# Performance work log

Measured on AMD Instinct MI355X. Metric: run time of the kernel, lower is better.

Reference implementation:

```python
import jax, jax.numpy as jnp
import numpy as np
from jax import lax

B, C, H, G = 128, 512, 14, 20  # batch, channels, feature-map size, num branches

# landmark indices for (point1, point2) of the 10 regions, and y-offset coefficients (x ruler)
_I1 = jnp.array([21, 18, 19, 41, 38, 49, 48, 51, 61, 56])
_I2 = jnp.array([22, 25, 24, 46, 43, 53, 54, 57, 63, 58])
_COEF = jnp.array([-0.5, -1.0 / 3.0, 1.0 / 3.0, 1.0, 0.0, 0.0, 0.0, 0.0, 0.0, 0.5], jnp.float32)


def process_landmarks(y):
    # y: [B,68,2] (x,y) pixel coords -> region_array [B,10,4] = (x1,y1,x2,y2)/16
    xl, yl = y[:, :, 0], y[:, :, 1]
    ruler = jnp.abs(xl[:, 39] - xl[:, 42])            # [B]
    off = ruler[:, None] * _COEF[None, :]             # [B,10]
    region = jnp.stack([xl[:, _I1], yl[:, _I1] + off, xl[:, _I2], yl[:, _I2] + off], axis=-1)
    return region / 16.0


def _crop(xi, cyi, cxi):
    # xi: [C,H,W]; 3x3 window centered at (cyi, cxi)
    z = jnp.asarray(0, cyi.dtype)
    return lax.dynamic_slice(xi, (z, cyi - 1, cxi - 1), (C, 3, 3))


def setup_inputs() -> dict:
    key = jax.random.key(0)
    ks = jax.random.split(key, 4)
    x = jax.random.normal(ks[0], (B, C, H, H), jnp.float32)
    y = jax.random.uniform(ks[1], (B, 68, 2), jnp.float32) * 224.0
    conv_w = jax.random.normal(ks[2], (G * C, C, 3, 3), jnp.float32) * 0.02  # grouped OIHW
    conv_b = jnp.zeros((G * C,), jnp.float32)
    fc_w = jax.random.normal(ks[3], (G, C * 36, 150), jnp.float32) * 0.01
    fc_b = jnp.zeros((G, 150), jnp.float32)
    return {"x": x, "y": y, "conv_w": conv_w, "conv_b": conv_b, "fc_w": fc_w, "fc_b": fc_b}


def reference(x, y, conv_w, conv_b, fc_w, fc_b):
    bsz = x.shape[0]
    pos = jnp.clip(process_landmarks(y).astype(jnp.int32), 1, 12)   # [B,10,4]
    cx = pos[:, :, jnp.array([0, 2])].reshape(bsz, G)               # [B,20] cols
    cy = pos[:, :, jnp.array([1, 3])].reshape(bsz, G)               # [B,20] rows
    crops = jax.vmap(jax.vmap(_crop, in_axes=(None, 0, 0)), in_axes=(0, 0, 0))(x, cy, cx)  # [B,20,C,3,3]
    new_input = crops.reshape(bsz, G * C, 3, 3)
    up = jax.image.resize(new_input, (bsz, G * C, 6, 6), method='bilinear')  # half-pixel, matches torch align_corners=False
    conv = lax.conv_general_dilated(up, conv_w, (1, 1), ((1, 1), (1, 1)),
                                    feature_group_count=G,
                                    dimension_numbers=('NCHW', 'OIHW', 'NCHW'))
    conv = jax.nn.relu(conv + conv_b[None, :, None, None])          # [B, G*C, 6, 6]
    feat = conv.reshape(bsz, G, C * 36)
    fc = jax.nn.relu(jnp.einsum('bgi,gio->bgo', feat, fc_w) + fc_b[None])  # [B,G,150]
    return fc.reshape(bsz, G * 150)
```

## Files before the change

### kernel.cpp

```cpp
#include <hip/hip_runtime.h>
#include <stdint.h>

#define B_  128
#define C_  512
#define G_  20
#define K2  4608
#define FCK 18432

typedef unsigned short u16;
typedef unsigned int   u32;
typedef __attribute__((ext_vector_type(8))) short  short8;
typedef __attribute__((ext_vector_type(4))) short  short4v;
typedef __attribute__((ext_vector_type(4))) float  float4v;

__device__ __forceinline__ u16 f2bf(float f) {
  u32 u = __builtin_bit_cast(u32, f);
  u = (u + 0x7fffu + ((u >> 16) & 1u)) >> 16;
  return (u16)u;
}

__device__ __forceinline__ void load_lds16(const void* g, void* l) {
  __builtin_amdgcn_global_load_lds(
      (const __attribute__((address_space(1))) void*)(uintptr_t)g,
      (__attribute__((address_space(3))) void*)(uint32_t)(uintptr_t)l,
      16, 0, 0);
}

#define BAR() __builtin_amdgcn_s_barrier()

__global__ void k_pos(const float* __restrict__ y, int* __restrict__ cx, int* __restrict__ cy) {
  int b = blockIdx.x * blockDim.x + threadIdx.x;
  if (b >= B_) return;
  const int   I1[10] = {21,18,19,41,38,49,48,51,61,56};
  const int   I2[10] = {22,25,24,46,43,53,54,57,63,58};
  const float CF[10] = {-0.5f, -1.0f/3.0f, 1.0f/3.0f, 1.0f, 0.f,0.f,0.f,0.f,0.f, 0.5f};
  const float* yb = y + b * 136;
  float ruler = fabsf(yb[2*39] - yb[2*42]);
  for (int j = 0; j < 10; ++j) {
    float off = ruler * CF[j];
    float vx1 = yb[2*I1[j]];
    float vy1 = yb[2*I1[j]+1] + off;
    float vx2 = yb[2*I2[j]];
    float vy2 = yb[2*I2[j]+1] + off;
    int px1 = (int)(vx1 * 0.0625f); px1 = min(max(px1,1),12);
    int py1 = (int)(vy1 * 0.0625f); py1 = min(max(py1,1),12);
    int px2 = (int)(vx2 * 0.0625f); px2 = min(max(px2,1),12);
    int py2 = (int)(vy2 * 0.0625f); py2 = min(max(py2,1),12);
    cx[b*20 + 2*j]   = px1;  cx[b*20 + 2*j+1] = px2;
    cy[b*20 + 2*j]   = py1;  cy[b*20 + 2*j+1] = py2;
  }
}

__global__ void __launch_bounds__(256) k_convw(const float* __restrict__ w, u16* __restrict__ wb) {
  __shared__ u16 lds[4 * 4608];
  int ob = blockIdx.x * 4;
  int tid = threadIdx.x;
  const float4* in4 = (const float4*)(w + (size_t)ob * 4608);
  #pragma unroll
  for (int r = 0; r < 18; ++r) {
    int fi = r * 256 + tid;
    float4 v = in4[fi];
    u16 q[4] = { f2bf(v.x), f2bf(v.y), f2bf(v.z), f2bf(v.w) };
    *(short4v*)&lds[fi * 4] = *(short4v*)q;
  }
  __syncthreads();
  #pragma unroll
  for (int r = 0; r < 9; ++r) {
    int wi = r * 256 + tid;
    int ci0 = (wi & 63) * 8;
    int t   = (wi >> 6) % 9;
    int o   = wi / 576;
    u16 vals[8];
    #pragma unroll
    for (int j = 0; j < 8; ++j) vals[j] = lds[o * 4608 + (ci0 + j) * 9 + t];
    *(short8*)(wb + ((size_t)(ob + o)) * K2 + t * 512 + ci0) = *(short8*)vals;
  }
}

__global__ void __launch_bounds__(256) k_up3(const float* __restrict__ x,
                                             const int* __restrict__ cx,
                                             const int* __restrict__ cy,
                                             u16* __restrict__ up3) {
  __shared__ float crop[3][3][C_];
  int bg = blockIdx.x;
  int b = bg / 20, g = bg % 20;
  int X = cx[bg] - 1, Y = cy[bg] - 1;
  const float* xb = x + (size_t)b * (C_*14*14);
  int t = threadIdx.x;
  for (int it = 0; it < 6; ++it) {
    int idx = it*256 + t;
    int r = idx >> 9, ci = idx & 511;
    const float* srow = xb + ci*196 + (Y + r)*14 + X;
    crop[r][0][ci] = srow[0];
    crop[r][1][ci] = srow[1];
    crop[r][2][ci] = srow[2];
  }
  __syncthreads();
  const int   R0[6] = {0,0,0,1,1,1};
  const float WA[6] = {1.f, .75f, .25f, .75f, .25f, 0.f};
  u16* dstbase = up3 + ((size_t)g*B_ + b) * 64 * C_;
  for (int it = 0; it < 16; ++it) {
    int cidx = it*256 + t;
    int pp = cidx >> 6;
    int c8 = (cidx & 63) * 8;
    int ph = pp >> 3, pw = pp & 7;
    u16 outv[8];
    if (ph == 0 || ph == 7 || pw == 0 || pw == 7) {
      #pragma unroll
      for (int j = 0; j < 8; ++j) outv[j] = 0;
    } else {
      int oh = ph - 1, ow = pw - 1;
      int r0 = R0[oh]; float wy0 = WA[oh], wy1 = 1.f - WA[oh];
      int s0 = R0[ow]; float wx0 = WA[ow], wx1 = 1.f - WA[ow];
      #pragma unroll
      for (int j = 0; j < 8; ++j) {
        int ci = c8 + j;
        float v = wy0*(wx0*crop[r0][s0][ci]   + wx1*crop[r0][s0+1][ci])
                + wy1*(wx0*crop[r0+1][s0][ci] + wx1*crop[r0+1][s0+1][ci]);
        outv[j] = f2bf(v);
      }
    }
    *(short8*)(dstbase + (size_t)pp*C_ + c8) = *(short8*)outv;
  }
}

__global__ void __launch_bounds__(512, 2) k_conv(const u16* __restrict__ wb,
                                                 const u16* __restrict__ up3,
                                                 const float* __restrict__ conv_b,
                                                 u16* __restrict__ feat) {
  __shared__ __align__(16) u16 As[2 * 256 * 64];
  __shared__ __align__(16) u16 Bs[2 * 256 * 64];
  int bid = blockIdx.x;
  int lid = (bid & 7) * 90 + (bid >> 3);
  int mt = lid & 1;
  int nt = (lid >> 1) % 18;
  int g  = lid / 36;
  int tid = threadIdx.x;
  int lane = tid & 63;
  int w = tid >> 6;
  int wr = w >> 2, wc = w & 3;
  int l15 = lane & 15, l4 = lane >> 4;

  int rl0 = tid >> 3, sl0 = tid & 7;
  const u16* srcA0 = wb + (size_t)(g*512 + mt*256 + rl0) * K2 + (sl0 ^ (rl0 & 7)) * 8;
  const u16* srcB[2][2];
  #pragma unroll
  for (int h = 0; h < 2; ++h)
    #pragma unroll
    for (int j = 0; j < 2; ++j) {
      int rl = j * 64 + rl0;
      int n  = nt * 256 + h * 128 + rl;
      unsigned bb = (unsigned)n / 36u;
      unsigned pix = (unsigned)n % 36u;
      int pixA = (int)(pix / 6u) * 8 + (int)(pix % 6u);
      srcB[h][j] = up3 + (((size_t)g*B_ + bb)*64 + pixA) * C_ + (sl0 ^ (rl0 & 7)) * 8;
    }

  auto stageA = [&](int st, int h) {
    if (st >= 72) return;
    int db = st & 1;
    size_t ko = (size_t)st * 64;
    #pragma unroll
    for (int j = 0; j < 2; ++j)
      load_lds16(srcA0 + (size_t)(h*128 + j*64) * K2 + ko,
                 (char*)As + db*32768 + h*16384 + (j*512 + tid)*16);
  };
  auto stageB = [&](int st, int h) {
    if (st >= 72) return;
    int db = st & 1;
    int t9 = st >> 3;
    size_t ko = (size_t)((t9/3)*8 + (t9%3)) * C_ + (size_t)(st & 7) * 64;
    #pragma unroll
    for (int j = 0; j < 2; ++j)
      load_lds16(srcB[h][j] + ko,
                 (char*)Bs + db*32768 + h*16384 + (j*512 + tid)*16);
  };

  auto ldfrag = [&](const char* base, int row, int kb) -> short8 {
    int cb = (kb*64 + l4*16) ^ ((row & 7) << 4);
    return *(const short8*)(base + row*128 + cb);
  };

  float4v acc[8][4];
  #pragma unroll
  for (int mi = 0; mi < 8; ++mi)
    #pragma unroll
    for (int nj = 0; nj < 4; ++nj) acc[mi][nj] = (float4v){0.f,0.f,0.f,0.f};

  stageB(0,0); stageB(0,1); stageA(0,0); stageA(0,1);
  stageB(1,0); stageB(1,1); stageA(1,0); stageA(1,1);
  asm volatile("s_waitcnt vmcnt(8)" ::: "memory");
  BAR();

  short8 aF[4][2], b01[2][2], b23[2][2];

#define LDA_HALF(BASE, MH)                                        \
  _Pragma("unroll") for (int mi = 0; mi < 4; ++mi)                \
    _Pragma("unroll") for (int kb = 0; kb < 2; ++kb)              \
      aF[mi][kb] = ldfrag(BASE, wr*128 + ((MH)*4 + mi)*16 + l15, kb);
#define LDB_HALF(BASE, NH, DST)                                   \
  _Pragma("unroll") for (int nj = 0; nj < 2; ++nj)                \
    _Pragma("unroll") for (int kb = 0; kb < 2; ++kb)              \
      DST[nj][kb] = ldfrag(BASE, wc*64 + ((NH)*2 + nj)*16 + l15, kb);
#define MFMA_QUAD(BF, QM, QN)                                     \
  __builtin_amdgcn_s_setprio(1);                                  \
  _Pragma("unroll") for (int kb = 0; kb < 2; ++kb)                \
    _Pragma("unroll") for (int mi = 0; mi < 4; ++mi)              \
      _Pragma("unroll") for (int nj = 0; nj < 2; ++nj)            \
        acc[(QM)*4+mi][(QN)*2+nj] = __builtin_amdgcn_mfma_f32_16x16x32_bf16( \
            aF[mi][kb], BF[nj][kb], acc[(QM)*4+mi][(QN)*2+nj], 0, 0, 0);     \
  __builtin_amdgcn_s_setprio(0);

  for (int it = 0; it < 36; ++it) {
    int t0 = 2 * it;
    const char* A0 = (const char*)As;
    const char* B0 = (const char*)Bs;
    const char* A1 = (const char*)As + 32768;
    const char* B1 = (const char*)Bs + 32768;
    LDA_HALF(A0, 0); LDB_HALF(B0, 0, b01);
    BAR(); MFMA_QUAD(b01, 0, 0); BAR();
    LDB_HALF(B0, 1, b23);
    BAR(); MFMA_QUAD(b23, 0, 1); BAR();
    LDA_HALF(A0, 1);
    stageB(t0 + 2, 0);
    BAR(); MFMA_QUAD(b01, 1, 0); BAR();
    stageB(t0 + 2, 1); stageA(t0 + 2, 0);
    BAR(); MFMA_QUAD(b23, 1, 1);
    if (it < 35) { asm volatile("s_waitcnt vmcnt(6)" ::: "memory"); }
    else         { asm volatile("s_waitcnt vmcnt(0)" ::: "memory"); }
    BAR();
    LDA_HALF(A1, 0); LDB_HALF(B1, 0, b01);
    stageA(t0 + 2, 1);
    BAR(); MFMA_QUAD(b01, 0, 0); BAR();
    LDB_HALF(B1, 1, b23);
    BAR(); MFMA_QUAD(b23, 0, 1); BAR();
    LDA_HALF(A1, 1);
    stageB(t0 + 3, 0);
    BAR(); MFMA_QUAD(b01, 1, 0); BAR();
    stageB(t0 + 3, 1); stageA(t0 + 3, 0); stageA(t0 + 3, 1);
    BAR(); MFMA_QUAD(b23, 1, 1);
    asm volatile("s_waitcnt vmcnt(8)" ::: "memory");
    BAR();
  }
#undef LDA_HALF
#undef LDB_HALF
#undef MFMA_QUAD

  float bias[8][4];
  #pragma unroll
  for (int mi = 0; mi < 8; ++mi)
    #pragma unroll
    for (int r = 0; r < 4; ++r)
      bias[mi][r] = conv_b[g*512 + mt*256 + wr*128 + mi*16 + l4*4 + r];
  #pragma unroll
  for (int nj = 0; nj < 4; ++nj) {
    int n = nt*256 + wc*64 + nj*16 + l15;
    unsigned bb = (unsigned)n / 36u;
    unsigned pix = (unsigned)n % 36u;
    size_t base = ((size_t)g*B_ + bb)*FCK + pix;
    #pragma unroll
    for (int mi = 0; mi < 8; ++mi)
      #pragma unroll
      for (int r = 0; r < 4; ++r) {
        int m = mt*256 + wr*128 + mi*16 + l4*4 + r;
        float v = fmaxf(acc[mi][nj][r] + bias[mi][r], 0.f);
        feat[base + (size_t)m*36] = f2bf(v);
      }
  }
}

__global__ void __launch_bounds__(256) k_fc(const u16* __restrict__ feat,
                                            const float* __restrict__ fw,
                                            float* __restrict__ accum) {
  __shared__ __align__(16) u16 As[128*64];
  __shared__ __align__(16) u16 Bs[160*64];
  int sp = blockIdx.x;
  int g  = blockIdx.y;
  int tid = threadIdx.x;
  int lane = tid & 63, w = tid >> 6;
  int wr = w >> 1, wc = w & 1;
  int rl = lane >> 3, s = lane & 7;
  int l15 = lane & 15, l4 = lane >> 4;

  const u16* gA[4]; u16* lA[4];
  #pragma unroll
  for (int i = 0; i < 4; ++i) {
    int r = w*32 + i*8 + rl;
    int c = s ^ (r & 7);
    gA[i] = feat + ((size_t)g*B_ + r)*FCK + c*8;
    lA[i] = (u16*)As + (w*32 + i*8) * 64;
  }

  float4v acc[4][5];
  #pragma unroll
  for (int mi = 0; mi < 4; ++mi)
    #pragma unroll
    for (int nj = 0; nj < 5; ++nj) acc[mi][nj] = (float4v){0.f,0.f,0.f,0.f};

  int kbase = sp * 576;
  for (int stp = 0; stp < 9; ++stp) {
    int i0 = kbase + stp * 64;
    __syncthreads();
    #pragma unroll
    for (int i = 0; i < 4; ++i) load_lds16(gA[i] + i0, lA[i]);
    #pragma unroll
    for (int bit = 0; bit < 5; ++bit) {
      int idx = bit * 256 + tid;
      int il8 = idx / 160;
      int o   = idx - il8 * 160;
      u16 vals[8];
      if (o < 150) {
        const float* src = fw + ((size_t)g * FCK + i0 + il8 * 8) * 150 + o;
        #pragma unroll
        for (int j = 0; j < 8; ++j) vals[j] = f2bf(src[(size_t)j * 150]);
      } else {
        #pragma unroll
        for (int j = 0; j < 8; ++j) vals[j] = 0;
      }
      *(short8*)((char*)Bs + o * 128 + ((il8 ^ (o & 7)) * 16)) = *(short8*)vals;
    }
    __syncthreads();

    short8 a[4][2], bf[5][2];
    #pragma unroll
    for (int kb = 0; kb < 2; ++kb) {
      #pragma unroll
      for (int mi = 0; mi < 4; ++mi) {
        int row = wr*64 + mi*16 + l15;
        int cb  = (kb*64 + l4*16) ^ ((row & 7) << 4);
        a[mi][kb] = *(const short8*)((const char*)As + row*128 + cb);
      }
      #pragma unroll
      for (int nj = 0; nj < 5; ++nj) {
        int row = wc*80 + nj*16 + l15;
        int cb  = (kb*64 + l4*16) ^ ((row & 7) << 4);
        bf[nj][kb] = *(const short8*)((const char*)Bs + row*128 + cb);
      }
    }
    #pragma unroll
    for (int kb = 0; kb < 2; ++kb)
      #pragma unroll
      for (int mi = 0; mi < 4; ++mi)
        #pragma unroll
        for (int nj = 0; nj < 5; ++nj)
          acc[mi][nj] = __builtin_amdgcn_mfma_f32_16x16x32_bf16(
              a[mi][kb], bf[nj][kb], acc[mi][nj], 0, 0, 0);
  }

  #pragma unroll
  for (int mi = 0; mi < 4; ++mi)
    #pragma unroll
    for (int r = 0; r < 4; ++r) {
      int brow = wr*64 + mi*16 + l4*4 + r;
      #pragma unroll
      for (int nj = 0; nj < 5; ++nj) {
        int o = wc*80 + nj*16 + l15;
        atomicAdd(&accum[((size_t)brow*20 + g)*160 + o], acc[mi][nj][r]);
      }
    }
}

__global__ void k_final(const float* __restrict__ accum, const float* __restrict__ fcb,
                        float* __restrict__ out) {
  int idx = blockIdx.x * 256 + threadIdx.x;
  if (idx >= B_*3000) return;
  unsigned b = (unsigned)idx / 3000u;
  unsigned rem = (unsigned)idx % 3000u;
  unsigned g = rem / 150u, o = rem % 150u;
  out[idx] = fmaxf(accum[((size_t)b*20 + g)*160 + o] + fcb[g*150 + o], 0.f);
}

extern "C" void kernel_launch(void* const* d_in, const int* in_sizes, int n_in,
                              void* d_out, int out_size, void* d_ws, size_t ws_size,
                              hipStream_t stream) {
  const float* x      = (const float*)d_in[0];
  const float* y      = (const float*)d_in[1];
  const float* conv_w = (const float*)d_in[2];
  const float* conv_b = (const float*)d_in[3];
  const float* fc_w   = (const float*)d_in[4];
  const float* fc_b   = (const float*)d_in[5];
  float* out = (float*)d_out;

  char* ws = (char*)d_ws;
  size_t off = 0;
  u16* Wb   = (u16*)(ws + off); off += (size_t)10240 * K2 * 2;
  u16* up3  = (u16*)(ws + off); off += (size_t)G_ * B_ * 64 * C_ * 2;
  u16* feat = (u16*)(ws + off); off += (size_t)G_ * B_ * FCK * 2;
  float* accum = (float*)(ws + off); off += (size_t)B_ * G_ * 160 * 4;
  int* cx = (int*)(ws + off); off += B_ * G_ * 4;
  int* cy = (int*)(ws + off); off += B_ * G_ * 4;

  k_pos<<<1, 128, 0, stream>>>(y, cx, cy);
  k_convw<<<2560, 256, 0, stream>>>(conv_w, Wb);
  k_up3<<<B_*G_, 256, 0, stream>>>(x, cx, cy, up3);
  hipMemsetAsync(accum, 0, (size_t)B_ * G_ * 160 * 4, stream);
  k_conv<<<720, 512, 0, stream>>>(Wb, up3, conv_b, feat);
  k_fc<<<dim3(32, 20), 256, 0, stream>>>(feat, fc_w, accum);
  k_final<<<(B_*3000 + 255)/256, 256, 0, stream>>>(accum, fc_b, out);
}
```

Measured before the change: 615.8 us.

## Store conv features pixel-major and merge weight-convert with crop-upsample kernel

After: 603.6 us. 2.0% less time.

```diff
diff --git a/kernel.cpp b/kernel.cpp
--- a/kernel.cpp
+++ b/kernel.cpp
@@ -51,76 +51,76 @@
   }
 }
 
-__global__ void __launch_bounds__(256) k_convw(const float* __restrict__ w, u16* __restrict__ wb) {
-  __shared__ u16 lds[4 * 4608];
-  int ob = blockIdx.x * 4;
+__global__ void __launch_bounds__(256) k_pre(const float* __restrict__ w, u16* __restrict__ wb,
+                                             const float* __restrict__ x,
+                                             const int* __restrict__ cx, const int* __restrict__ cy,
+                                             u16* __restrict__ up3) {
+  __shared__ __align__(16) char smraw[4 * 4608 * 2];
   int tid = threadIdx.x;
-  const float4* in4 = (const float4*)(w + (size_t)ob * 4608);
-  #pragma unroll
-  for (int r = 0; r < 18; ++r) {
-    int fi = r * 256 + tid;
-    float4 v = in4[fi];
-    u16 q[4] = { f2bf(v.x), f2bf(v.y), f2bf(v.z), f2bf(v.w) };
-    *(short4v*)&lds[fi * 4] = *(short4v*)q;
-  }
-  __syncthreads();
-  #pragma unroll
-  for (int r = 0; r < 9; ++r) {
-    int wi = r * 256 + tid;
-    int ci0 = (wi & 63) * 8;
-    int t   = (wi >> 6) % 9;
-    int o   = wi / 576;
-    u16 vals[8];
-    #pragma unroll
-    for (int j = 0; j < 8; ++j) vals[j] = lds[o * 4608 + (ci0 + j) * 9 + t];
-    *(short8*)(wb + ((size_t)(ob + o)) * K2 + t * 512 + ci0) = *(short8*)vals;
-  }
-}
-
-__global__ void __launch_bounds__(256) k_up3(const float* __restrict__ x,
-                                             const int* __restrict__ cx,
-                                             const int* __restrict__ cy,
-                                             u16* __restrict__ up3) {
-  __shared__ float crop[3][3][C_];
-  int bg = blockIdx.x;
-  int b = bg / 20, g = bg % 20;
-  int X = cx[bg] - 1, Y = cy[bg] - 1;
-  const float* xb = x + (size_t)b * (C_*14*14);
-  int t = threadIdx.x;
-  for (int it = 0; it < 6; ++it) {
-    int idx = it*256 + t;
-    int r = idx >> 9, ci = idx & 511;
-    const float* srow = xb + ci*196 + (Y + r)*14 + X;
-    crop[r][0][ci] = srow[0];
-    crop[r][1][ci] = srow[1];
-    crop[r][2][ci] = srow[2];
-  }
-  __syncthreads();
-  const int   R0[6] = {0,0,0,1,1,1};
-  const float WA[6] = {1.f, .75f, .25f, .75f, .25f, 0.f};
-  u16* dstbase = up3 + ((size_t)g*B_ + b) * 64 * C_;
-  for (int it = 0; it < 16; ++it) {
-    int cidx = it*256 + t;
-    int pp = cidx >> 6;
-    int c8 = (cidx & 63) * 8;
-    int ph = pp >> 3, pw = pp & 7;
-    u16 outv[8];
-    if (ph == 0 || ph == 7 || pw == 0 || pw == 7) {
-      #pragma unroll
-      for (int j = 0; j < 8; ++j) outv[j] = 0;
-    } else {
-      int oh = ph - 1, ow = pw - 1;
-      int r0 = R0[oh]; float wy0 = WA[oh], wy1 = 1.f - WA[oh];
-      int s0 = R0[ow]; float wx0 = WA[ow], wx1 = 1.f - WA[ow];
-      #pragma unroll
-      for (int j = 0; j < 8; ++j) {
-        int ci = c8 + j;
-        float v = wy0*(wx0*crop[r0][s0][ci]   + wx1*crop[r0][s0+1][ci])
-                + wy1*(wx0*crop[r0+1][s0][ci] + wx1*crop[r0+1][s0+1][ci]);
-        outv[j] = f2bf(v);
+  if (blockIdx.x < 2560) {
+    u16* lds = (u16*)smraw;
+    int ob = blockIdx.x * 4;
+    const float4* in4 = (const float4*)(w + (size_t)ob * 4608);
+    #pragma unroll
+    for (int r = 0; r < 18; ++r) {
+      int fi = r * 256 + tid;
+      float4 v = in4[fi];
+      u16 q[4] = { f2bf(v.x), f2bf(v.y), f2bf(v.z), f2bf(v.w) };
+      *(short4v*)&lds[fi * 4] = *(short4v*)q;
+    }
+    __syncthreads();
+    #pragma unroll
+    for (int r = 0; r < 9; ++r) {
+      int wi = r * 256 + tid;
+      int ci0 = (wi & 63) * 8;
+      int t   = (wi >> 6) % 9;
+      int o   = wi / 576;
+      u16 vals[8];
+      #pragma unroll
+      for (int j = 0; j < 8; ++j) vals[j] = lds[o * 4608 + (ci0 + j) * 9 + t];
+      *(short8*)(wb + ((size_t)(ob + o)) * K2 + t * 512 + ci0) = *(short8*)vals;
+    }
+  } else {
+    float (*crop)[3][C_] = (float(*)[3][C_])smraw;
+    int bg = blockIdx.x - 2560;
+    int b = bg / 20, g = bg % 20;
+    int X = cx[bg] - 1, Y = cy[bg] - 1;
+    const float* xb = x + (size_t)b * (C_*14*14);
+    for (int it = 0; it < 6; ++it) {
+      int idx = it*256 + tid;
+      int r = idx >> 9, ci = idx & 511;
+      const float* srow = xb + ci*196 + (Y + r)*14 + X;
+      crop[r][0][ci] = srow[0];
+      crop[r][1][ci] = srow[1];
+      crop[r][2][ci] = srow[2];
+    }
+    __syncthreads();
+    const int   R0[6] = {0,0,0,1,1,1};
+    const float WA[6] = {1.f, .75f, .25f, .75f, .25f, 0.f};
+    u16* dstbase = up3 + ((size_t)g*B_ + b) * 64 * C_;
+    for (int it = 0; it < 16; ++it) {
+      int cidx = it*256 + tid;
+      int pp = cidx >> 6;
+      int c8 = (cidx & 63) * 8;
+      int ph = pp >> 3, pw = pp & 7;
+      u16 outv[8];
+      if (ph == 0 || ph == 7 || pw == 0 || pw == 7) {
+        #pragma unroll
+        for (int j = 0; j < 8; ++j) outv[j] = 0;
+      } else {
+        int oh = ph - 1, ow = pw - 1;
+        int r0 = R0[oh]; float wy0 = WA[oh], wy1 = 1.f - WA[oh];
+        int s0 = R0[ow]; float wx0 = WA[ow], wx1 = 1.f - WA[ow];
+        #pragma unroll
+        for (int j = 0; j < 8; ++j) {
+          int ci = c8 + j;
+          float v = wy0*(wx0*crop[r0][s0][ci]   + wx1*crop[r0][s0+1][ci])
+                  + wy1*(wx0*crop[r0+1][s0][ci] + wx1*crop[r0+1][s0+1][ci]);
+          outv[j] = f2bf(v);
+        }
       }
-    }
-    *(short8*)(dstbase + (size_t)pp*C_ + c8) = *(short8*)outv;
+      *(short8*)(dstbase + (size_t)pp*C_ + c8) = *(short8*)outv;
+    }
   }
 }
 
@@ -257,15 +257,16 @@
     int n = nt*256 + wc*64 + nj*16 + l15;
     unsigned bb = (unsigned)n / 36u;
     unsigned pix = (unsigned)n % 36u;
-    size_t base = ((size_t)g*B_ + bb)*FCK + pix;
-    #pragma unroll
-    for (int mi = 0; mi < 8; ++mi)
-      #pragma unroll
-      for (int r = 0; r < 4; ++r) {
-        int m = mt*256 + wr*128 + mi*16 + l4*4 + r;
-        float v = fmaxf(acc[mi][nj][r] + bias[mi][r], 0.f);
-        feat[base + (size_t)m*36] = f2bf(v);
-      }
+    size_t base = ((size_t)g*B_ + bb)*FCK + (size_t)pix*512;
+    #pragma unroll
+    for (int mi = 0; mi < 8; ++mi) {
+      int co0 = mt*256 + wr*128 + mi*16 + l4*4;
+      u16 q[4];
+      #pragma unroll
+      for (int r = 0; r < 4; ++r)
+        q[r] = f2bf(fmaxf(acc[mi][nj][r] + bias[mi][r], 0.f));
+      *(short4v*)(feat + base + co0) = *(short4v*)q;
+    }
   }
 }
 
@@ -300,6 +301,8 @@
   int kbase = sp * 576;
   for (int stp = 0; stp < 9; ++stp) {
     int i0 = kbase + stp * 64;
+    int pix = i0 >> 9;
+    int cobase = i0 & 511;
     __syncthreads();
     #pragma unroll
     for (int i = 0; i < 4; ++i) load_lds16(gA[i] + i0, lA[i]);
@@ -310,9 +313,9 @@
       int o   = idx - il8 * 160;
       u16 vals[8];
       if (o < 150) {
-        const float* src = fw + ((size_t)g * FCK + i0 + il8 * 8) * 150 + o;
+        const float* src = fw + ((size_t)g * FCK + (size_t)(cobase + il8 * 8) * 36 + pix) * 150 + o;
         #pragma unroll
-        for (int j = 0; j < 8; ++j) vals[j] = f2bf(src[(size_t)j * 150]);
+        for (int j = 0; j < 8; ++j) vals[j] = f2bf(src[(size_t)j * 5400]);
       } else {
         #pragma unroll
         for (int j = 0; j < 8; ++j) vals[j] = 0;
@@ -391,9 +394,8 @@
   int* cy = (int*)(ws + off); off += B_ * G_ * 4;
 
   k_pos<<<1, 128, 0, stream>>>(y, cx, cy);
-  k_convw<<<2560, 256, 0, stream>>>(conv_w, Wb);
-  k_up3<<<B_*G_, 256, 0, stream>>>(x, cx, cy, up3);
   hipMemsetAsync(accum, 0, (size_t)B_ * G_ * 160 * 4, stream);
+  k_pre<<<5120, 256, 0, stream>>>(conv_w, Wb, x, cx, cy, up3);
   k_conv<<<720, 512, 0, stream>>>(Wb, up3, conv_b, feat);
   k_fc<<<dim3(32, 20), 256, 0, stream>>>(feat, fc_w, accum);
   k_final<<<(B_*3000 + 255)/256, 256, 0, stream>>>(accum, fc_b, out);
```
